# Performance work log

Hardware: AMD Instinct MI355X
Metric: run time of the kernel (lower is better)

## Reference

```python
import jax, jax.numpy as jnp
import numpy as np

B, N, KEY_DIM, VALUE_DIM, INNER_DIM, HEADS = 2, 4096, 512, 512, 512, 8
DIM_HEAD = INNER_DIM // HEADS
LN_EPS = 1e-5


def _layernorm(x, gamma, beta):
    mu = jnp.mean(x, axis=-1, keepdims=True)
    xc = x - mu
    var = jnp.mean(xc * xc, axis=-1, keepdims=True)
    return xc * jax.lax.rsqrt(var + LN_EPS) * gamma + beta


def setup_inputs() -> dict:
    key = jax.random.key(0)
    ks = jax.random.split(key, 8)
    keys = jax.random.normal(ks[0], (B, N, KEY_DIM), dtype=jnp.float32)
    values = jax.random.normal(ks[1], (B, N, VALUE_DIM), dtype=jnp.float32)
    mask = jax.random.randint(ks[2], (B, N), 0, 2).astype(jnp.bool_)
    W_qk = jax.random.normal(ks[3], (KEY_DIM, 2 * INNER_DIM), dtype=jnp.float32) * 0.02
    W_v = jax.random.normal(ks[4], (VALUE_DIM, INNER_DIM), dtype=jnp.float32) * 0.02
    W_out = jax.random.normal(ks[5], (INNER_DIM, VALUE_DIM), dtype=jnp.float32) * 0.02
    b_out = jnp.zeros((VALUE_DIM,), dtype=jnp.float32)
    qk_gamma = jnp.ones((KEY_DIM,), dtype=jnp.float32)
    qk_beta = jnp.zeros((KEY_DIM,), dtype=jnp.float32)
    v_gamma = jnp.ones((VALUE_DIM,), dtype=jnp.float32)
    v_beta = jnp.zeros((VALUE_DIM,), dtype=jnp.float32)
    return {"keys": keys, "values": values, "mask": mask,
            "qk_gamma": qk_gamma, "qk_beta": qk_beta,
            "v_gamma": v_gamma, "v_beta": v_beta,
            "W_qk": W_qk, "W_v": W_v, "W_out": W_out, "b_out": b_out}


def reference(keys, values, mask, qk_gamma, qk_beta, v_gamma, v_beta, W_qk, W_v, W_out, b_out):
    # LayerNorms on inputs
    kn = _layernorm(keys, qk_gamma, qk_beta)          # [B,N,KEY_DIM]
    vn = _layernorm(values, v_gamma, v_beta)          # [B,N,VALUE_DIM]
    # joint q/k projection, no bias
    qk = kn @ W_qk                                    # [B,N,2*INNER]
    q, k = qk[..., :INNER_DIM], qk[..., INNER_DIM:]
    # split heads: b n (h d) -> b h n d
    q = q.reshape(B, N, HEADS, DIM_HEAD).transpose(0, 2, 1, 3)
    k = k.reshape(B, N, HEADS, DIM_HEAD).transpose(0, 2, 1, 3)
    v = (vn @ W_v).reshape(B, N, HEADS, DIM_HEAD).transpose(0, 2, 1, 3)
    # clamp then scaled QK^T (AttentionMap math)
    q = jnp.clip(q, -5.0, 5.0)
    k = jnp.clip(k, -5.0, 5.0)
    scale = DIM_HEAD ** -0.5
    dots = jnp.einsum("bhqd,bhkd->bhqk", q, k) * scale  # [B,H,N,N]
    # mask: True keys are not attended to; broadcast (B,N)->(B,1,1,N)
    dots = jnp.where(mask[:, None, None, :], -jnp.inf, dots)
    attn = jax.nn.softmax(dots, axis=-1)
    out = jnp.einsum("bhqk,bhkd->bhqd", attn, v)       # [B,H,N,D]
    out = out.transpose(0, 2, 1, 3).reshape(B, N, INNER_DIM)
    return out @ W_out + b_out                         # [B,N,VALUE_DIM]
```

## Files before the change

kernel.cpp:

```cpp
#include <hip/hip_runtime.h>
#include <stdint.h>

typedef float f32x4 __attribute__((ext_vector_type(4)));
typedef float f32x16 __attribute__((ext_vector_type(16)));
typedef short s16x8 __attribute__((ext_vector_type(8)));
typedef int i32x4 __attribute__((ext_vector_type(4)));

typedef const __attribute__((address_space(1))) uint32_t* gas_t;
typedef __attribute__((address_space(3))) uint32_t* las_t;

__device__ __forceinline__ void gload16(const void* g, void* l) {
  __builtin_amdgcn_global_load_lds((gas_t)g, (las_t)l, 16, 0, 0);
}

__device__ __forceinline__ short f2bf(float f) {
  union { float f; uint32_t u; } v; v.f = f;
  uint32_t r = v.u + 0x7fffu + ((v.u >> 16) & 1u);
  return (short)(r >> 16);
}

__device__ __forceinline__ uint32_t cvtpk_bf16(float lo, float hi) {
  uint32_t r;
  asm("v_cvt_pk_bf16_f32 %0, %1, %2" : "=v"(r) : "v"(lo), "v"(hi));
  return r;
}

__device__ __forceinline__ void perm32swap(uint32_t& a, uint32_t& b) {
  asm("v_permlane32_swap_b32 %0, %1" : "+v"(a), "+v"(b));
}

#define MFMA16(a,b,c) __builtin_amdgcn_mfma_f32_16x16x32_bf16((a),(b),(c),0,0,0)
#define MFMA32(a,b,c) __builtin_amdgcn_mfma_f32_32x32x16_bf16((a),(b),(c),0,0,0)

__global__ void mask_detect_kernel(const uint32_t* __restrict__ m, uint32_t* __restrict__ flag) {
  uint32_t v = m[blockIdx.x * 256 + threadIdx.x];
  if (v > 1u) atomicOr(flag, 1u);
}

__global__ __launch_bounds__(256) void scan_kernel(const uint32_t* __restrict__ m,
    const uint32_t* __restrict__ flag, int* __restrict__ idx, int* __restrict__ cnts) {
  __shared__ int wt[4];
  const int b = blockIdx.x, t = threadIdx.x;
  const int lane = t & 63, w = t >> 6;
  const uint32_t f = *flag;
  int v[16]; int s = 0;
  if (f) {
    uint4 raw = ((const uint4*)((const uint8_t*)m + (size_t)b * 4096))[t];
    uint32_t ws_[4] = {raw.x, raw.y, raw.z, raw.w};
#pragma unroll
    for (int e = 0; e < 16; e++)
      v[e] = (((ws_[e >> 2] >> ((e & 3) * 8)) & 0xffu) == 0) ? 1 : 0;
  } else {
#pragma unroll
    for (int j = 0; j < 4; j++) {
      uint4 raw = ((const uint4*)(m + (size_t)b * 4096))[t * 4 + j];
      v[j * 4 + 0] = (raw.x == 0); v[j * 4 + 1] = (raw.y == 0);
      v[j * 4 + 2] = (raw.z == 0); v[j * 4 + 3] = (raw.w == 0);
    }
  }
#pragma unroll
  for (int e = 0; e < 16; e++) s += v[e];
  int sc = s;
#pragma unroll
  for (int off = 1; off < 64; off <<= 1) {
    int y = __shfl_up(sc, off);
    if (lane >= off) sc += y;
  }
  if (lane == 63) wt[w] = sc;
  __syncthreads();
  int woff = 0;
#pragma unroll
  for (int i = 0; i < 4; i++) if (i < w) woff += wt[i];
  int base = woff + sc - s;
#pragma unroll
  for (int e = 0; e < 16; e++)
    if (v[e]) { idx[b * 4096 + base] = b * 4096 + t * 16 + e; base++; }
  const int cnt = wt[0] + wt[1] + wt[2] + wt[3];
  const int cpad = (cnt + 127) & ~127;
  for (int j = cnt + t; j < cpad; j += 256) idx[b * 4096 + j] = 8192;
  if (t == 0) { cnts[b * 2] = cnt; cnts[b * 2 + 1] = cpad; }
}

__global__ __launch_bounds__(256) void transpose_kernel(const float* __restrict__ W,
    short* __restrict__ WT, int R, int C) {
  __shared__ float tile[32][33];
  const int c0 = blockIdx.x * 32, r0 = blockIdx.y * 32;
  const int tx = threadIdx.x & 31, ty = threadIdx.x >> 5;
#pragma unroll
  for (int i = 0; i < 32; i += 8)
    tile[ty + i][tx] = W[(size_t)(r0 + ty + i) * C + c0 + tx];
  __syncthreads();
#pragma unroll
  for (int i = 0; i < 32; i += 8)
    WT[(size_t)(c0 + ty + i) * R + r0 + tx] = f2bf(tile[tx][ty + i]);
}

__global__ __launch_bounds__(64) void ln_kernel(const float* __restrict__ keys,
    const float* __restrict__ values, const float* __restrict__ g0, const float* __restrict__ b0,
    const float* __restrict__ g1, const float* __restrict__ b1,
    short* __restrict__ kn, short* __restrict__ vn) {
  const int row = blockIdx.x, sel = blockIdx.y, lane = threadIdx.x;
  short* out = (sel ? vn : kn) + (size_t)row * 512;
  if (row == 8192) {
    s16x8 z = (s16x8){0,0,0,0,0,0,0,0};
    *(s16x8*)(out + lane * 8) = z;
    return;
  }
  const float* x = (sel ? values : keys) + (size_t)row * 512;
  const float* ga = sel ? g1 : g0;
  const float* be = sel ? b1 : b0;
  float4 a = ((const float4*)x)[lane * 2];
  float4 c = ((const float4*)x)[lane * 2 + 1];
  float s = a.x + a.y + a.z + a.w + c.x + c.y + c.z + c.w;
  float sq = a.x*a.x + a.y*a.y + a.z*a.z + a.w*a.w + c.x*c.x + c.y*c.y + c.z*c.z + c.w*c.w;
#pragma unroll
  for (int m = 1; m < 64; m <<= 1) { s += __shfl_xor(s, m); sq += __shfl_xor(sq, m); }
  float mu = s * (1.0f / 512.0f);
  float var = sq * (1.0f / 512.0f) - mu * mu;
  float rs = rsqrtf(var + 1e-5f);
  float xs[8] = {a.x, a.y, a.z, a.w, c.x, c.y, c.z, c.w};
  s16x8 o;
#pragma unroll
  for (int j = 0; j < 8; j++)
    o[j] = f2bf((xs[j] - mu) * rs * ga[lane * 8 + j] + be[lane * 8 + j]);
  *(s16x8*)(out + lane * 8) = o;
}

__device__ __forceinline__ void gemm_core(const short* __restrict__ A,
                                          const short* __restrict__ BT,
                                          int row0, int col0,
                                          short* ldsA, short* ldsB,
                                          f32x4 acc[4][4]) {
  const int t = threadIdx.x;
  const int lane = t & 63, w = t >> 6;
  const int wr = w >> 1, wc = w & 1;
  const int l15 = lane & 15, l4 = lane >> 4;
#pragma unroll
  for (int mi = 0; mi < 4; mi++)
#pragma unroll
    for (int ni = 0; ni < 4; ni++) acc[mi][ni] = (f32x4){0.f, 0.f, 0.f, 0.f};

  for (int k0 = 0; k0 < 512; k0 += 64) {
    __syncthreads();
#pragma unroll
    for (int i = 0; i < 4; i++) {
      int q = i * 256 + t;
      int row = q >> 3, ch = q & 7;
      int chs = ch ^ (row & 7);
      gload16(A + (size_t)(row0 + row) * 512 + k0 + chs * 8, ldsA + (i * 256 + w * 64) * 8);
      gload16(BT + (size_t)(col0 + row) * 512 + k0 + chs * 8, ldsB + (i * 256 + w * 64) * 8);
    }
    __syncthreads();
#pragma unroll
    for (int kk = 0; kk < 2; kk++) {
      s16x8 af[4], bf[4];
#pragma unroll
      for (int mi = 0; mi < 4; mi++) {
        int row = wr * 64 + mi * 16 + l15;
        int ch = (kk * 4 + l4) ^ (row & 7);
        af[mi] = *(const s16x8*)(ldsA + row * 64 + ch * 8);
      }
#pragma unroll
      for (int ni = 0; ni < 4; ni++) {
        int row = wc * 64 + ni * 16 + l15;
        int ch = (kk * 4 + l4) ^ (row & 7);
        bf[ni] = *(const s16x8*)(ldsB + row * 64 + ch * 8);
      }
#pragma unroll
      for (int mi = 0; mi < 4; mi++)
#pragma unroll
        for (int ni = 0; ni < 4; ni++)
          acc[mi][ni] = MFMA16(af[mi], bf[ni], acc[mi][ni]);
    }
  }
}

__device__ __forceinline__ void gemm_core64(const short* __restrict__ A,
                                            const short* __restrict__ BT,
                                            int row0, int col0,
                                            short* ldsA, short* ldsB,
                                            f32x4 acc[4][2]) {
  const int t = threadIdx.x;
  const int lane = t & 63, w = t >> 6;
  const int wr = w >> 1, wc = w & 1;
  const int l15 = lane & 15, l4 = lane >> 4;
#pragma unroll
  for (int mi = 0; mi < 4; mi++)
#pragma unroll
    for (int ni = 0; ni < 2; ni++) acc[mi][ni] = (f32x4){0.f, 0.f, 0.f, 0.f};

  for (int k0 = 0; k0 < 512; k0 += 64) {
    __syncthreads();
#pragma unroll
    for (int i = 0; i < 4; i++) {
      int q = i * 256 + t;
      int row = q >> 3, ch = q & 7;
      int chs = ch ^ (row & 7);
      gload16(A + (size_t)(row0 + row) * 512 + k0 + chs * 8, ldsA + (i * 256 + w * 64) * 8);
    }
#pragma unroll
    for (int i = 0; i < 2; i++) {
      int q = i * 256 + t;
      int row = q >> 3, ch = q & 7;
      int chs = ch ^ (row & 7);
      gload16(BT + (size_t)(col0 + row) * 512 + k0 + chs * 8, ldsB + (i * 256 + w * 64) * 8);
    }
    __syncthreads();
#pragma unroll
    for (int kk = 0; kk < 2; kk++) {
      s16x8 af[4], bf[2];
#pragma unroll
      for (int mi = 0; mi < 4; mi++) {
        int row = wr * 64 + mi * 16 + l15;
        int ch = (kk * 4 + l4) ^ (row & 7);
        af[mi] = *(const s16x8*)(ldsA + row * 64 + ch * 8);
      }
#pragma unroll
      for (int ni = 0; ni < 2; ni++) {
        int row = wc * 32 + ni * 16 + l15;
        int ch = (kk * 4 + l4) ^ (row & 7);
        bf[ni] = *(const s16x8*)(ldsB + row * 64 + ch * 8);
      }
#pragma unroll
      for (int mi = 0; mi < 4; mi++)
#pragma unroll
        for (int ni = 0; ni < 2; ni++)
          acc[mi][ni] = MFMA16(af[mi], bf[ni], acc[mi][ni]);
    }
  }
}

__device__ __forceinline__ void gemm_core_idx(const short* __restrict__ A,
                                              const short* __restrict__ BT,
                                              const int* __restrict__ idxp,
                                              int row0, int col0,
                                              short* ldsA, short* ldsB,
                                              f32x4 acc[4][4]) {
  const int t = threadIdx.x;
  const int lane = t & 63, w = t >> 6;
  const int wr = w >> 1, wc = w & 1;
  const int l15 = lane & 15, l4 = lane >> 4;
  int arow[4];
#pragma unroll
  for (int i = 0; i < 4; i++)
    arow[i] = idxp[row0 + ((i * 256 + t) >> 3)];
#pragma unroll
  for (int mi = 0; mi < 4; mi++)
#pragma unroll
    for (int ni = 0; ni < 4; ni++) acc[mi][ni] = (f32x4){0.f, 0.f, 0.f, 0.f};

  for (int k0 = 0; k0 < 512; k0 += 64) {
    __syncthreads();
#pragma unroll
    for (int i = 0; i < 4; i++) {
      int q = i * 256 + t;
      int row = q >> 3, ch = q & 7;
      int chs = ch ^ (row & 7);
      gload16(A + (size_t)arow[i] * 512 + k0 + chs * 8, ldsA + (i * 256 + w * 64) * 8);
      gload16(BT + (size_t)(col0 + row) * 512 + k0 + chs * 8, ldsB + (i * 256 + w * 64) * 8);
    }
    __syncthreads();
#pragma unroll
    for (int kk = 0; kk < 2; kk++) {
      s16x8 af[4], bf[4];
#pragma unroll
      for (int mi = 0; mi < 4; mi++) {
        int row = wr * 64 + mi * 16 + l15;
        int ch = (kk * 4 + l4) ^ (row & 7);
        af[mi] = *(const s16x8*)(ldsA + row * 64 + ch * 8);
      }
#pragma unroll
      for (int ni = 0; ni < 4; ni++) {
        int row = wc * 64 + ni * 16 + l15;
        int ch = (kk * 4 + l4) ^ (row & 7);
        bf[ni] = *(const s16x8*)(ldsB + row * 64 + ch * 8);
      }
#pragma unroll
      for (int mi = 0; mi < 4; mi++)
#pragma unroll
        for (int ni = 0; ni < 4; ni++)
          acc[mi][ni] = MFMA16(af[mi], bf[ni], acc[mi][ni]);
    }
  }
}

__global__ __launch_bounds__(256) void gemm_q_kernel(const short* __restrict__ kn,
    const short* __restrict__ WqkT, short* __restrict__ Qg) {
  __shared__ short ldsA[128 * 64], ldsB[64 * 64];
  f32x4 acc[4][2];
  const int bm = blockIdx.x, bn = blockIdx.y;
  gemm_core64(kn, WqkT, bm * 128, bn * 64, ldsA, ldsB, acc);
  const int t = threadIdx.x, lane = t & 63, w = t >> 6, wr = w >> 1, wc = w & 1;
  const int l15 = lane & 15, l4 = lane >> 4;
  const float QSCL = 0.125f * 1.44269504088896f;
#pragma unroll
  for (int mi = 0; mi < 4; mi++)
#pragma unroll
    for (int ni = 0; ni < 2; ni++) {
      int c = bn * 64 + wc * 32 + ni * 16 + l15;
      int h = c >> 6, d = c & 63;
#pragma unroll
      for (int r = 0; r < 4; r++) {
        int row = bm * 128 + wr * 64 + mi * 16 + l4 * 4 + r;
        int b = row >> 12, n = row & 4095;
        float v = acc[mi][ni][r];
        v = fminf(fmaxf(v, -5.0f), 5.0f) * QSCL;
        Qg[((size_t)((b * 8 + h) * 4096 + n) << 6) + d] = f2bf(v);
      }
    }
}

__global__ __launch_bounds__(256) void gemm_kv_kernel(const short* __restrict__ kn,
    const short* __restrict__ vn, const short* __restrict__ WqkT,
    const short* __restrict__ WvT, const int* __restrict__ idx,
    const int* __restrict__ cnts, short* __restrict__ Kg, short* __restrict__ VTg) {
  const int z = blockIdx.z, b = z & 1, isV = z >> 1;
  const int bm = blockIdx.x, bn = blockIdx.y;
  if (bm * 128 >= cnts[b * 2 + 1]) return;
  __shared__ short lds[2][128 * 64];
  f32x4 acc[4][4];
  const int t = threadIdx.x, lane = t & 63, w = t >> 6, wr = w >> 1, wc = w & 1;
  const int l15 = lane & 15, l4 = lane >> 4;
  if (!isV) {
    gemm_core_idx(kn, WqkT, idx + b * 4096, bm * 128, 512 + bn * 128, lds[0], lds[1], acc);
#pragma unroll
    for (int mi = 0; mi < 4; mi++)
#pragma unroll
      for (int ni = 0; ni < 4; ni++) {
        int c = bn * 128 + wc * 64 + ni * 16 + l15;
        int h = c >> 6, d = c & 63;
#pragma unroll
        for (int r = 0; r < 4; r++) {
          int j = bm * 128 + wr * 64 + mi * 16 + l4 * 4 + r;
          float v = acc[mi][ni][r];
          v = fminf(fmaxf(v, -5.0f), 5.0f);
          Kg[((size_t)((b * 8 + h) * 4096 + j) << 6) + d] = f2bf(v);
        }
      }
  } else {
    gemm_core_idx(vn, WvT, idx + b * 4096, bm * 128, bn * 128, lds[0], lds[1], acc);
    __syncthreads();
    short* T = (short*)lds;
#pragma unroll
    for (int mi = 0; mi < 4; mi++)
#pragma unroll
      for (int ni = 0; ni < 4; ni++) {
        int c_loc = wc * 64 + ni * 16 + l15;
#pragma unroll
        for (int r = 0; r < 4; r++) {
          int n_loc = wr * 64 + mi * 16 + l4 * 4 + r;
          T[c_loc * 128 + (((n_loc >> 3) ^ (c_loc & 15)) << 3) + (n_loc & 7)] = f2bf(acc[mi][ni][r]);
        }
      }
    __syncthreads();
#pragma unroll
    for (int jj = 0; jj < 8; jj++) {
      int c_loc = jj * 16 + (t >> 4);
      int nch = t & 15;
      s16x8 v = *(const s16x8*)(T + c_loc * 128 + ((nch ^ (c_loc & 15)) << 3));
      int cg = bn * 128 + c_loc, h = cg >> 6, d = cg & 63;
      int j = bm * 128 + nch * 8;
      *(s16x8*)(VTg + (size_t)((b * 8 + h) * 64 + d) * 4096 + j) = v;
    }
  }
}

__global__ __launch_bounds__(256) void gemm_out_kernel(const short* __restrict__ O,
    const short* __restrict__ WoutT, const float* __restrict__ bias, float* __restrict__ out) {
  __shared__ short ldsA[128 * 64], ldsB[64 * 64];
  f32x4 acc[4][2];
  const int bm = blockIdx.x, bn = blockIdx.y;
  gemm_core64(O, WoutT, bm * 128, bn * 64, ldsA, ldsB, acc);
  const int t = threadIdx.x, lane = t & 63, w = t >> 6, wr = w >> 1, wc = w & 1;
  const int l15 = lane & 15, l4 = lane >> 4;
#pragma unroll
  for (int ni = 0; ni < 2; ni++) {
    int col = bn * 64 + wc * 32 + ni * 16 + l15;
    float bv = bias[col];
#pragma unroll
    for (int mi = 0; mi < 4; mi++)
#pragma unroll
      for (int r = 0; r < 4; r++) {
        int row = bm * 128 + wr * 64 + mi * 16 + l4 * 4 + r;
        out[(size_t)row * 512 + col] = acc[mi][ni][r] + bv;
      }
  }
}

__global__ __launch_bounds__(512, 4) void attn_kernel(const short* __restrict__ Qg,
    const short* __restrict__ Kg, const short* __restrict__ VTg,
    const int* __restrict__ cnts, short* __restrict__ O) {
  __shared__ short smem[32768];
  short* KloB = smem;
  short* VloB = smem + 8192;
  short* KhiB = smem + 16384;
  short* VhiB = smem + 24576;

  const int bid = blockIdx.x;
  const int xcd = bid & 7, local = bid >> 3;
  const int bh = xcd * 2 + (local & 1);
  const int qb = local >> 1;
  const int b = bh >> 3, h = bh & 7;
  const int t = threadIdx.x, lane = t & 63, w = t >> 6;
  const int l31 = lane & 31, hh = lane >> 5;
  const int half = w >> 2, wq = w & 3;

  const short* Qp = Qg + (size_t)bh * 4096 * 64;
  const short* Kp = Kg + (size_t)bh * 4096 * 64;
  const short* Vp = VTg + (size_t)bh * 64 * 4096;

  const int cnt  = cnts[b * 2];
  const int cpad = cnts[b * 2 + 1];
  const int nit  = cpad >> 7;
  const int hb   = cpad >> 1;
  const int kbase = half ? hb : 0;

  const int qrow = qb * 128 + wq * 32 + l31;
  s16x8 qf[4];
#pragma unroll
  for (int dblk = 0; dblk < 4; dblk++)
    qf[dblk] = *(const s16x8*)(Qp + (size_t)qrow * 64 + dblk * 16 + hh * 8);

  f32x16 oac[2];
#pragma unroll
  for (int db = 0; db < 2; db++)
#pragma unroll
    for (int r = 0; r < 16; r++) oac[db][r] = 0.0f;
  float m_ = -60.0f, l_ = 0.0f;

  const short* KtS = half ? KhiB : KloB;
  const short* VtS = half ? VhiB : VloB;

  auto STAGE = [&](int buf, int i) {
    int row = t >> 3, ch = t & 7, chs = ch ^ (row & 7);
    gload16(Kp + (size_t)(i * 64 + row) * 64 + chs * 8,        KloB + buf * 4096 + w * 512);
    gload16(Kp + (size_t)(hb + i * 64 + row) * 64 + chs * 8,   KhiB + buf * 4096 + w * 512);
    gload16(Vp + (size_t)row * 4096 + i * 64 + chs * 8,        VloB + buf * 4096 + w * 512);
    gload16(Vp + (size_t)row * 4096 + hb + i * 64 + chs * 8,   VhiB + buf * 4096 + w * 512);
  };

  STAGE(0, 0);
  __syncthreads();

  for (int it = 0; it < nit; it++) {
    const int cur = it & 1;
    if (it < nit - 1) STAGE(cur ^ 1, it + 1);
    const short* Kt = KtS + cur * 4096;
    const int kb_t = kbase + it * 64;

    f32x16 sc[2];
    __builtin_amdgcn_s_setprio(1);
#pragma unroll
    for (int kb = 0; kb < 2; kb++) {
      f32x16 s_;
#pragma unroll
      for (int r = 0; r < 16; r++) s_[r] = 0.0f;
      const int krow = kb * 32 + l31;
#pragma unroll
      for (int dblk = 0; dblk < 4; dblk++) {
        int ch = (2 * dblk + hh) ^ (krow & 7);
        s16x8 kf = *(const s16x8*)(Kt + krow * 64 + ch * 8);
        s_ = MFMA32(kf, qf[dblk], s_);
      }
      sc[kb] = s_;
    }
    __builtin_amdgcn_s_setprio(0);

    if (kb_t + 64 > cnt) {
#pragma unroll
      for (int kb = 0; kb < 2; kb++)
#pragma unroll
        for (int r = 0; r < 16; r++) {
          int key = kb_t + kb * 32 + (r & 3) + 8 * (r >> 2) + 4 * hh;
          if (key >= cnt) sc[kb][r] = -1e30f;
        }
    }

    float mx0 = -1e30f, mx1 = -1e30f, mx2 = -1e30f, mx3 = -1e30f;
#pragma unroll
    for (int kb = 0; kb < 2; kb++)
#pragma unroll
      for (int r = 0; r < 16; r += 4) {
        mx0 = fmaxf(mx0, sc[kb][r + 0]);
        mx1 = fmaxf(mx1, sc[kb][r + 1]);
        mx2 = fmaxf(mx2, sc[kb][r + 2]);
        mx3 = fmaxf(mx3, sc[kb][r + 3]);
      }
    float mx = fmaxf(fmaxf(mx0, mx1), fmaxf(mx2, mx3));
    mx = fmaxf(mx, __shfl_xor(mx, 32));

    if (!__all(mx <= m_ + 5.0f)) {
      float mnew = fmaxf(m_, mx);
      float alpha = __builtin_amdgcn_exp2f(m_ - mnew);
      m_ = mnew;
      l_ *= alpha;
#pragma unroll
      for (int db = 0; db < 2; db++)
#pragma unroll
        for (int r = 0; r < 16; r++) oac[db][r] *= alpha;
    }

    float ls = 0.0f;
    uint32_t pw[4][4];
#pragma unroll
    for (int kb = 0; kb < 2; kb++) {
      float p[16];
#pragma unroll
      for (int r = 0; r < 16; r++) {
        p[r] = __builtin_amdgcn_exp2f(sc[kb][r] - m_);
        ls += p[r];
      }
#pragma unroll
      for (int ksl = 0; ksl < 2; ksl++) {
        const int fi = kb * 2 + ksl, b0 = ksl * 8;
        uint32_t a0 = cvtpk_bf16(p[b0 + 0], p[b0 + 1]);
        uint32_t b0w = cvtpk_bf16(p[b0 + 4], p[b0 + 5]);
        perm32swap(a0, b0w);
        uint32_t a1 = cvtpk_bf16(p[b0 + 2], p[b0 + 3]);
        uint32_t b1w = cvtpk_bf16(p[b0 + 6], p[b0 + 7]);
        perm32swap(a1, b1w);
        pw[fi][0] = a0; pw[fi][1] = a1; pw[fi][2] = b0w; pw[fi][3] = b1w;
      }
    }
    ls += __shfl_xor(ls, 32);
    l_ += ls;

    __builtin_amdgcn_s_setprio(1);
#pragma unroll
    for (int db = 0; db < 2; db++) {
      const int d = db * 32 + l31;
#pragma unroll
      for (int ks = 0; ks < 4; ks++) {
        int ch = (2 * ks + hh) ^ (d & 7);
        s16x8 vf = *(const s16x8*)(VtS + cur * 4096 + d * 64 + ch * 8);
        i32x4 pv = {(int)pw[ks][0], (int)pw[ks][1], (int)pw[ks][2], (int)pw[ks][3]};
        oac[db] = MFMA32(vf, __builtin_bit_cast(s16x8, pv), oac[db]);
      }
    }
    __builtin_amdgcn_s_setprio(0);

    __syncthreads();
  }

  float* mrg = (float*)smem;
  float* ml  = mrg + 8192;
  if (half) {
#pragma unroll
    for (int db = 0; db < 2; db++)
#pragma unroll
      for (int r = 0; r < 16; r++)
        mrg[wq * 2048 + (db * 16 + r) * 64 + lane] = oac[db][r];
    ml[wq * 128 + lane * 2]     = m_;
    ml[wq * 128 + lane * 2 + 1] = l_;
  }
  __syncthreads();
  if (!half) {
    float m2 = ml[wq * 128 + lane * 2];
    float l2 = ml[wq * 128 + lane * 2 + 1];
    float mF = fmaxf(m_, m2);
    float e1 = __builtin_amdgcn_exp2f(m_ - mF);
    float e2 = __builtin_amdgcn_exp2f(m2 - mF);
    l_ = l_ * e1 + l2 * e2;
#pragma unroll
    for (int db = 0; db < 2; db++)
#pragma unroll
      for (int r = 0; r < 16; r++)
        oac[db][r] = oac[db][r] * e1 + mrg[wq * 2048 + (db * 16 + r) * 64 + lane] * e2;

    float inv = 1.0f / l_;
    short* epi = smem + 17408 + wq * 2048;
#pragma unroll
    for (int db = 0; db < 2; db++)
#pragma unroll
      for (int g = 0; g < 4; g++) {
        uint32_t w0 = cvtpk_bf16(oac[db][g * 4 + 0] * inv, oac[db][g * 4 + 1] * inv);
        uint32_t w1 = cvtpk_bf16(oac[db][g * 4 + 2] * inv, oac[db][g * 4 + 3] * inv);
        int chunk = db * 4 + g;
        uint2* dst = (uint2*)((char*)epi + l31 * 128 + ((chunk ^ (l31 & 7)) << 4) + hh * 8);
        *dst = make_uint2(w0, w1);
      }
#pragma unroll
    for (int i = 0; i < 4; i++) {
      int c = hh * 4 + i;
      s16x8 v = *(const s16x8*)((char*)epi + l31 * 128 + ((c ^ (l31 & 7)) << 4));
      *(s16x8*)(O + ((size_t)(b * 4096 + qrow) * 512) + h * 64 + c * 8) = v;
    }
  }
}

extern "C" void kernel_launch(void* const* d_in, const int* in_sizes, int n_in,
                              void* d_out, int out_size, void* d_ws, size_t ws_size,
                              hipStream_t stream) {
  const float* keys     = (const float*)d_in[0];
  const float* values   = (const float*)d_in[1];
  const uint32_t* maskp = (const uint32_t*)d_in[2];
  const float* qk_gamma = (const float*)d_in[3];
  const float* qk_beta  = (const float*)d_in[4];
  const float* v_gamma  = (const float*)d_in[5];
  const float* v_beta   = (const float*)d_in[6];
  const float* W_qk     = (const float*)d_in[7];
  const float* W_v      = (const float*)d_in[8];
  const float* W_out    = (const float*)d_in[9];
  const float* b_out    = (const float*)d_in[10];
  float* out = (float*)d_out;
  char* ws = (char*)d_ws;
  const size_t MB = 1u << 20;
  short* kn    = (short*)(ws);
  short* vn    = (short*)(ws + 9 * MB);
  short* Qg    = (short*)(ws + 18 * MB);
  short* Kg    = (short*)(ws + 26 * MB);
  short* VTg   = (short*)(ws + 34 * MB);
  short* O     = (short*)(ws + 42 * MB);
  short* WqkT  = (short*)(ws + 50 * MB);
  short* WvT   = (short*)(ws + 51 * MB);
  short* WoutT = (short*)(ws + 51 * MB + 512 * 1024);
  int*   idx   = (int*)(ws + 52 * MB);
  int*   cnts  = (int*)(ws + 52 * MB + 32 * 1024);
  uint32_t* flag = (uint32_t*)(ws + 52 * MB + 33 * 1024);

  hipMemsetAsync(flag, 0, 4, stream);
  mask_detect_kernel<<<8, 256, 0, stream>>>(maskp, flag);
  scan_kernel<<<2, 256, 0, stream>>>(maskp, flag, idx, cnts);
  transpose_kernel<<<dim3(32, 16), 256, 0, stream>>>(W_qk, WqkT, 512, 1024);
  transpose_kernel<<<dim3(16, 16), 256, 0, stream>>>(W_v, WvT, 512, 512);
  transpose_kernel<<<dim3(16, 16), 256, 0, stream>>>(W_out, WoutT, 512, 512);
  ln_kernel<<<dim3(8193, 2), 64, 0, stream>>>(keys, values, qk_gamma, qk_beta, v_gamma, v_beta, kn, vn);
  gemm_q_kernel<<<dim3(64, 8), 256, 0, stream>>>(kn, WqkT, Qg);
  gemm_kv_kernel<<<dim3(32, 4, 4), 256, 0, stream>>>(kn, vn, WqkT, WvT, idx, cnts, Kg, VTg);
  attn_kernel<<<512, 512, 0, stream>>>(Qg, Kg, VTg, cnts, O);
  gemm_out_kernel<<<dim3(64, 8), 256, 0, stream>>>(O, WoutT, b_out, out);
}
```

Before: 110.8 us.

## Merge prep launches into one kernel and fuse Q/KV projection kernels

Folds mask detection, the mask scan, the three weight transposes and both LayerNorms into a single prep_kernel launch that dispatches on block index. LayerNorm rows are now handled by four waves per 256-thread block instead of one 64-thread block each. Mask-type detection becomes a per-block ballot in place of a memset plus an atomic kernel. The Q projection and the masked K/V projections share one proj_kernel launch. The goal is to cut launch count and inter-kernel gaps, at the cost of a heterogeneous grid whose branches have different register and LDS needs.

```diff
diff --git a/kernel.cpp b/kernel.cpp
--- a/kernel.cpp
+++ b/kernel.cpp
@@ -32,146 +32,111 @@
 #define MFMA16(a,b,c) __builtin_amdgcn_mfma_f32_16x16x32_bf16((a),(b),(c),0,0,0)
 #define MFMA32(a,b,c) __builtin_amdgcn_mfma_f32_32x32x16_bf16((a),(b),(c),0,0,0)
 
-__global__ void mask_detect_kernel(const uint32_t* __restrict__ m, uint32_t* __restrict__ flag) {
-  uint32_t v = m[blockIdx.x * 256 + threadIdx.x];
-  if (v > 1u) atomicOr(flag, 1u);
-}
-
-__global__ __launch_bounds__(256) void scan_kernel(const uint32_t* __restrict__ m,
-    const uint32_t* __restrict__ flag, int* __restrict__ idx, int* __restrict__ cnts) {
+__global__ __launch_bounds__(256) void prep_kernel(
+    const uint32_t* __restrict__ maskp,
+    const float* __restrict__ W_qk, const float* __restrict__ W_v,
+    const float* __restrict__ W_out,
+    short* __restrict__ WqkT, short* __restrict__ WvT, short* __restrict__ WoutT,
+    const float* __restrict__ keys, const float* __restrict__ values,
+    const float* __restrict__ g0, const float* __restrict__ b0,
+    const float* __restrict__ g1, const float* __restrict__ b1,
+    short* __restrict__ kn, short* __restrict__ vn,
+    int* __restrict__ idx, int* __restrict__ cnts) {
+  __shared__ float tile[32][33];
   __shared__ int wt[4];
-  const int b = blockIdx.x, t = threadIdx.x;
+  __shared__ int wdet[4];
+  const int bid = blockIdx.x, t = threadIdx.x;
   const int lane = t & 63, w = t >> 6;
-  const uint32_t f = *flag;
-  int v[16]; int s = 0;
-  if (f) {
-    uint4 raw = ((const uint4*)((const uint8_t*)m + (size_t)b * 4096))[t];
-    uint32_t ws_[4] = {raw.x, raw.y, raw.z, raw.w};
+
+  if (bid < 2) {
+    const int b = bid;
+    uint4 probe = ((const uint4*)maskp)[t];
+    bool big = (probe.x > 1u) || (probe.y > 1u) || (probe.z > 1u) || (probe.w > 1u);
+    unsigned long long bal = __ballot(big);
+    if (lane == 0) wdet[w] = (bal != 0ull) ? 1 : 0;
+    __syncthreads();
+    const int f = wdet[0] | wdet[1] | wdet[2] | wdet[3];
+
+    int v[16]; int s = 0;
+    if (f) {
+      uint4 raw = ((const uint4*)((const uint8_t*)maskp + (size_t)b * 4096))[t];
+      uint32_t ws_[4] = {raw.x, raw.y, raw.z, raw.w};
+#pragma unroll
+      for (int e = 0; e < 16; e++)
+        v[e] = (((ws_[e >> 2] >> ((e & 3) * 8)) & 0xffu) == 0) ? 1 : 0;
+    } else {
+#pragma unroll
+      for (int j = 0; j < 4; j++) {
+        uint4 raw = ((const uint4*)(maskp + (size_t)b * 4096))[t * 4 + j];
+        v[j * 4 + 0] = (raw.x == 0); v[j * 4 + 1] = (raw.y == 0);
+        v[j * 4 + 2] = (raw.z == 0); v[j * 4 + 3] = (raw.w == 0);
+      }
+    }
+#pragma unroll
+    for (int e = 0; e < 16; e++) s += v[e];
+    int sc = s;
+#pragma unroll
+    for (int off = 1; off < 64; off <<= 1) {
+      int y = __shfl_up(sc, off);
+      if (lane >= off) sc += y;
+    }
+    if (lane == 63) wt[w] = sc;
+    __syncthreads();
+    int woff = 0;
+#pragma unroll
+    for (int i = 0; i < 4; i++) if (i < w) woff += wt[i];
+    int base = woff + sc - s;
 #pragma unroll
     for (int e = 0; e < 16; e++)
-      v[e] = (((ws_[e >> 2] >> ((e & 3) * 8)) & 0xffu) == 0) ? 1 : 0;
+      if (v[e]) { idx[b * 4096 + base] = b * 4096 + t * 16 + e; base++; }
+    const int cnt = wt[0] + wt[1] + wt[2] + wt[3];
+    const int cpad = (cnt + 127) & ~127;
+    for (int j = cnt + t; j < cpad; j += 256) idx[b * 4096 + j] = 8192;
+    if (t == 0) { cnts[b * 2] = cnt; cnts[b * 2 + 1] = cpad; }
+  } else if (bid < 1026) {
+    int job = bid - 2;
+    const float* W; short* WT; int C;
+    if (job < 512)       { W = W_qk;  WT = WqkT;  C = 1024; }
+    else if (job < 768)  { job -= 512; W = W_v;   WT = WvT;  C = 512; }
+    else                 { job -= 768; W = W_out; WT = WoutT; C = 512; }
+    const int tx_ = C >> 5;
+    const int c0 = (job % tx_) * 32, r0 = (job / tx_) * 32;
+    const int tx = t & 31, ty = t >> 5;
+#pragma unroll
+    for (int i = 0; i < 32; i += 8)
+      tile[ty + i][tx] = W[(size_t)(r0 + ty + i) * C + c0 + tx];
+    __syncthreads();
+#pragma unroll
+    for (int i = 0; i < 32; i += 8)
+      WT[(size_t)(c0 + ty + i) * 512 + r0 + tx] = f2bf(tile[tx][ty + i]);
   } else {
-#pragma unroll
-    for (int j = 0; j < 4; j++) {
-      uint4 raw = ((const uint4*)(m + (size_t)b * 4096))[t * 4 + j];
-      v[j * 4 + 0] = (raw.x == 0); v[j * 4 + 1] = (raw.y == 0);
-      v[j * 4 + 2] = (raw.z == 0); v[j * 4 + 3] = (raw.w == 0);
-    }
-  }
-#pragma unroll
-  for (int e = 0; e < 16; e++) s += v[e];
-  int sc = s;
-#pragma unroll
-  for (int off = 1; off < 64; off <<= 1) {
-    int y = __shfl_up(sc, off);
-    if (lane >= off) sc += y;
-  }
-  if (lane == 63) wt[w] = sc;
-  __syncthreads();
-  int woff = 0;
-#pragma unroll
-  for (int i = 0; i < 4; i++) if (i < w) woff += wt[i];
-  int base = woff + sc - s;
-#pragma unroll
-  for (int e = 0; e < 16; e++)
-    if (v[e]) { idx[b * 4096 + base] = b * 4096 + t * 16 + e; base++; }
-  const int cnt = wt[0] + wt[1] + wt[2] + wt[3];
-  const int cpad = (cnt + 127) & ~127;
-  for (int j = cnt + t; j < cpad; j += 256) idx[b * 4096 + j] = 8192;
-  if (t == 0) { cnts[b * 2] = cnt; cnts[b * 2 + 1] = cpad; }
-}
-
-__global__ __launch_bounds__(256) void transpose_kernel(const float* __restrict__ W,
-    short* __restrict__ WT, int R, int C) {
-  __shared__ float tile[32][33];
-  const int c0 = blockIdx.x * 32, r0 = blockIdx.y * 32;
-  const int tx = threadIdx.x & 31, ty = threadIdx.x >> 5;
-#pragma unroll
-  for (int i = 0; i < 32; i += 8)
-    tile[ty + i][tx] = W[(size_t)(r0 + ty + i) * C + c0 + tx];
-  __syncthreads();
-#pragma unroll
-  for (int i = 0; i < 32; i += 8)
-    WT[(size_t)(c0 + ty + i) * R + r0 + tx] = f2bf(tile[tx][ty + i]);
-}
-
-__global__ __launch_bounds__(64) void ln_kernel(const float* __restrict__ keys,
-    const float* __restrict__ values, const float* __restrict__ g0, const float* __restrict__ b0,
-    const float* __restrict__ g1, const float* __restrict__ b1,
-    short* __restrict__ kn, short* __restrict__ vn) {
-  const int row = blockIdx.x, sel = blockIdx.y, lane = threadIdx.x;
-  short* out = (sel ? vn : kn) + (size_t)row * 512;
-  if (row == 8192) {
-    s16x8 z = (s16x8){0,0,0,0,0,0,0,0};
-    *(s16x8*)(out + lane * 8) = z;
-    return;
-  }
-  const float* x = (sel ? values : keys) + (size_t)row * 512;
-  const float* ga = sel ? g1 : g0;
-  const float* be = sel ? b1 : b0;
-  float4 a = ((const float4*)x)[lane * 2];
-  float4 c = ((const float4*)x)[lane * 2 + 1];
-  float s = a.x + a.y + a.z + a.w + c.x + c.y + c.z + c.w;
-  float sq = a.x*a.x + a.y*a.y + a.z*a.z + a.w*a.w + c.x*c.x + c.y*c.y + c.z*c.z + c.w*c.w;
-#pragma unroll
-  for (int m = 1; m < 64; m <<= 1) { s += __shfl_xor(s, m); sq += __shfl_xor(sq, m); }
-  float mu = s * (1.0f / 512.0f);
-  float var = sq * (1.0f / 512.0f) - mu * mu;
-  float rs = rsqrtf(var + 1e-5f);
-  float xs[8] = {a.x, a.y, a.z, a.w, c.x, c.y, c.z, c.w};
-  s16x8 o;
-#pragma unroll
-  for (int j = 0; j < 8; j++)
-    o[j] = f2bf((xs[j] - mu) * rs * ga[lane * 8 + j] + be[lane * 8 + j]);
-  *(s16x8*)(out + lane * 8) = o;
-}
-
-__device__ __forceinline__ void gemm_core(const short* __restrict__ A,
-                                          const short* __restrict__ BT,
-                                          int row0, int col0,
-                                          short* ldsA, short* ldsB,
-                                          f32x4 acc[4][4]) {
-  const int t = threadIdx.x;
-  const int lane = t & 63, w = t >> 6;
-  const int wr = w >> 1, wc = w & 1;
-  const int l15 = lane & 15, l4 = lane >> 4;
-#pragma unroll
-  for (int mi = 0; mi < 4; mi++)
-#pragma unroll
-    for (int ni = 0; ni < 4; ni++) acc[mi][ni] = (f32x4){0.f, 0.f, 0.f, 0.f};
-
-  for (int k0 = 0; k0 < 512; k0 += 64) {
-    __syncthreads();
-#pragma unroll
-    for (int i = 0; i < 4; i++) {
-      int q = i * 256 + t;
-      int row = q >> 3, ch = q & 7;
-      int chs = ch ^ (row & 7);
-      gload16(A + (size_t)(row0 + row) * 512 + k0 + chs * 8, ldsA + (i * 256 + w * 64) * 8);
-      gload16(BT + (size_t)(col0 + row) * 512 + k0 + chs * 8, ldsB + (i * 256 + w * 64) * 8);
-    }
-    __syncthreads();
-#pragma unroll
-    for (int kk = 0; kk < 2; kk++) {
-      s16x8 af[4], bf[4];
-#pragma unroll
-      for (int mi = 0; mi < 4; mi++) {
-        int row = wr * 64 + mi * 16 + l15;
-        int ch = (kk * 4 + l4) ^ (row & 7);
-        af[mi] = *(const s16x8*)(ldsA + row * 64 + ch * 8);
-      }
-#pragma unroll
-      for (int ni = 0; ni < 4; ni++) {
-        int row = wc * 64 + ni * 16 + l15;
-        int ch = (kk * 4 + l4) ^ (row & 7);
-        bf[ni] = *(const s16x8*)(ldsB + row * 64 + ch * 8);
-      }
-#pragma unroll
-      for (int mi = 0; mi < 4; mi++)
-#pragma unroll
-        for (int ni = 0; ni < 4; ni++)
-          acc[mi][ni] = MFMA16(af[mi], bf[ni], acc[mi][ni]);
-    }
+    int job = (bid - 1026) * 4 + w;
+    if (job >= 16386) return;
+    const int sel = job & 1, row = job >> 1;
+    short* out = (sel ? vn : kn) + (size_t)row * 512;
+    if (row == 8192) {
+      s16x8 z = (s16x8){0,0,0,0,0,0,0,0};
+      *(s16x8*)(out + lane * 8) = z;
+      return;
+    }
+    const float* x = (sel ? values : keys) + (size_t)row * 512;
+    const float* ga = sel ? g1 : g0;
+    const float* be = sel ? b1 : b0;
+    float4 a = ((const float4*)x)[lane * 2];
+    float4 c = ((const float4*)x)[lane * 2 + 1];
+    float s = a.x + a.y + a.z + a.w + c.x + c.y + c.z + c.w;
+    float sq = a.x*a.x + a.y*a.y + a.z*a.z + a.w*a.w + c.x*c.x + c.y*c.y + c.z*c.z + c.w*c.w;
+#pragma unroll
+    for (int m = 1; m < 64; m <<= 1) { s += __shfl_xor(s, m); sq += __shfl_xor(sq, m); }
+    float mu = s * (1.0f / 512.0f);
+    float var = sq * (1.0f / 512.0f) - mu * mu;
+    float rs = rsqrtf(var + 1e-5f);
+    float xs[8] = {a.x, a.y, a.z, a.w, c.x, c.y, c.z, c.w};
+    s16x8 o;
+#pragma unroll
+    for (int j = 0; j < 8; j++)
+      o[j] = f2bf((xs[j] - mu) * rs * ga[lane * 8 + j] + be[lane * 8 + j]);
+    *(s16x8*)(out + lane * 8) = o;
   }
 }
 
@@ -284,83 +249,83 @@
   }
 }
 
-__global__ __launch_bounds__(256) void gemm_q_kernel(const short* __restrict__ kn,
-    const short* __restrict__ WqkT, short* __restrict__ Qg) {
-  __shared__ short ldsA[128 * 64], ldsB[64 * 64];
-  f32x4 acc[4][2];
-  const int bm = blockIdx.x, bn = blockIdx.y;
-  gemm_core64(kn, WqkT, bm * 128, bn * 64, ldsA, ldsB, acc);
+__global__ __launch_bounds__(256) void proj_kernel(const short* __restrict__ kn,
+    const short* __restrict__ vn, const short* __restrict__ WqkT,
+    const short* __restrict__ WvT, const int* __restrict__ idx,
+    const int* __restrict__ cnts, short* __restrict__ Qg,
+    short* __restrict__ Kg, short* __restrict__ VTg) {
+  __shared__ short lds[2][128 * 64];
+  const int bid = blockIdx.x;
   const int t = threadIdx.x, lane = t & 63, w = t >> 6, wr = w >> 1, wc = w & 1;
   const int l15 = lane & 15, l4 = lane >> 4;
-  const float QSCL = 0.125f * 1.44269504088896f;
-#pragma unroll
-  for (int mi = 0; mi < 4; mi++)
-#pragma unroll
-    for (int ni = 0; ni < 2; ni++) {
-      int c = bn * 64 + wc * 32 + ni * 16 + l15;
-      int h = c >> 6, d = c & 63;
-#pragma unroll
-      for (int r = 0; r < 4; r++) {
-        int row = bm * 128 + wr * 64 + mi * 16 + l4 * 4 + r;
-        int b = row >> 12, n = row & 4095;
-        float v = acc[mi][ni][r];
-        v = fminf(fmaxf(v, -5.0f), 5.0f) * QSCL;
-        Qg[((size_t)((b * 8 + h) * 4096 + n) << 6) + d] = f2bf(v);
-      }
-    }
-}
-
-__global__ __launch_bounds__(256) void gemm_kv_kernel(const short* __restrict__ kn,
-    const short* __restrict__ vn, const short* __restrict__ WqkT,
-    const short* __restrict__ WvT, const int* __restrict__ idx,
-    const int* __restrict__ cnts, short* __restrict__ Kg, short* __restrict__ VTg) {
-  const int z = blockIdx.z, b = z & 1, isV = z >> 1;
-  const int bm = blockIdx.x, bn = blockIdx.y;
-  if (bm * 128 >= cnts[b * 2 + 1]) return;
-  __shared__ short lds[2][128 * 64];
-  f32x4 acc[4][4];
-  const int t = threadIdx.x, lane = t & 63, w = t >> 6, wr = w >> 1, wc = w & 1;
-  const int l15 = lane & 15, l4 = lane >> 4;
-  if (!isV) {
-    gemm_core_idx(kn, WqkT, idx + b * 4096, bm * 128, 512 + bn * 128, lds[0], lds[1], acc);
+
+  if (bid < 512) {
+    const int bm = bid >> 3, bn = bid & 7;
+    f32x4 acc[4][2];
+    gemm_core64(kn, WqkT, bm * 128, bn * 64, lds[0], lds[1], acc);
+    const float QSCL = 0.125f * 1.44269504088896f;
 #pragma unroll
     for (int mi = 0; mi < 4; mi++)
 #pragma unroll
-      for (int ni = 0; ni < 4; ni++) {
-        int c = bn * 128 + wc * 64 + ni * 16 + l15;
+      for (int ni = 0; ni < 2; ni++) {
+        int c = bn * 64 + wc * 32 + ni * 16 + l15;
         int h = c >> 6, d = c & 63;
 #pragma unroll
         for (int r = 0; r < 4; r++) {
-          int j = bm * 128 + wr * 64 + mi * 16 + l4 * 4 + r;
+          int row = bm * 128 + wr * 64 + mi * 16 + l4 * 4 + r;
+          int b = row >> 12, n = row & 4095;
           float v = acc[mi][ni][r];
-          v = fminf(fmaxf(v, -5.0f), 5.0f);
-          Kg[((size_t)((b * 8 + h) * 4096 + j) << 6) + d] = f2bf(v);
+          v = fminf(fmaxf(v, -5.0f), 5.0f) * QSCL;
+          Qg[((size_t)((b * 8 + h) * 4096 + n) << 6) + d] = f2bf(v);
         }
       }
   } else {
-    gemm_core_idx(vn, WvT, idx + b * 4096, bm * 128, bn * 128, lds[0], lds[1], acc);
-    __syncthreads();
-    short* T = (short*)lds;
-#pragma unroll
-    for (int mi = 0; mi < 4; mi++)
-#pragma unroll
-      for (int ni = 0; ni < 4; ni++) {
-        int c_loc = wc * 64 + ni * 16 + l15;
-#pragma unroll
-        for (int r = 0; r < 4; r++) {
-          int n_loc = wr * 64 + mi * 16 + l4 * 4 + r;
-          T[c_loc * 128 + (((n_loc >> 3) ^ (c_loc & 15)) << 3) + (n_loc & 7)] = f2bf(acc[mi][ni][r]);
+    const int b2 = bid - 512;
+    const int bm = b2 >> 4, bn = (b2 >> 2) & 3, z = b2 & 3;
+    const int b = z & 1, isV = z >> 1;
+    if (bm * 128 >= cnts[b * 2 + 1]) return;
+    f32x4 acc[4][4];
+    if (!isV) {
+      gemm_core_idx(kn, WqkT, idx + b * 4096, bm * 128, 512 + bn * 128, lds[0], lds[1], acc);
+#pragma unroll
+      for (int mi = 0; mi < 4; mi++)
+#pragma unroll
+        for (int ni = 0; ni < 4; ni++) {
+          int c = bn * 128 + wc * 64 + ni * 16 + l15;
+          int h = c >> 6, d = c & 63;
+#pragma unroll
+          for (int r = 0; r < 4; r++) {
+            int j = bm * 128 + wr * 64 + mi * 16 + l4 * 4 + r;
+            float v = acc[mi][ni][r];
+            v = fminf(fmaxf(v, -5.0f), 5.0f);
+            Kg[((size_t)((b * 8 + h) * 4096 + j) << 6) + d] = f2bf(v);
+          }
         }
-      }
-    __syncthreads();
-#pragma unroll
-    for (int jj = 0; jj < 8; jj++) {
-      int c_loc = jj * 16 + (t >> 4);
-      int nch = t & 15;
-      s16x8 v = *(const s16x8*)(T + c_loc * 128 + ((nch ^ (c_loc & 15)) << 3));
-      int cg = bn * 128 + c_loc, h = cg >> 6, d = cg & 63;
-      int j = bm * 128 + nch * 8;
-      *(s16x8*)(VTg + (size_t)((b * 8 + h) * 64 + d) * 4096 + j) = v;
+    } else {
+      gemm_core_idx(vn, WvT, idx + b * 4096, bm * 128, bn * 128, lds[0], lds[1], acc);
+      __syncthreads();
+      short* T = (short*)lds;
+#pragma unroll
+      for (int mi = 0; mi < 4; mi++)
+#pragma unroll
+        for (int ni = 0; ni < 4; ni++) {
+          int c_loc = wc * 64 + ni * 16 + l15;
+#pragma unroll
+          for (int r = 0; r < 4; r++) {
+            int n_loc = wr * 64 + mi * 16 + l4 * 4 + r;
+            T[c_loc * 128 + (((n_loc >> 3) ^ (c_loc & 15)) << 3) + (n_loc & 7)] = f2bf(acc[mi][ni][r]);
+          }
+        }
+      __syncthreads();
+#pragma unroll
+      for (int jj = 0; jj < 8; jj++) {
+        int c_loc = jj * 16 + (t >> 4);
+        int nch = t & 15;
+        s16x8 v = *(const s16x8*)(T + c_loc * 128 + ((nch ^ (c_loc & 15)) << 3));
+        int cg = bn * 128 + c_loc, h = cg >> 6, d = cg & 63;
+        int j = bm * 128 + nch * 8;
+        *(s16x8*)(VTg + (size_t)((b * 8 + h) * 64 + d) * 4096 + j) = v;
+      }
     }
   }
 }
@@ -616,17 +581,11 @@
   short* WoutT = (short*)(ws + 51 * MB + 512 * 1024);
   int*   idx   = (int*)(ws + 52 * MB);
   int*   cnts  = (int*)(ws + 52 * MB + 32 * 1024);
-  uint32_t* flag = (uint32_t*)(ws + 52 * MB + 33 * 1024);
-
-  hipMemsetAsync(flag, 0, 4, stream);
-  mask_detect_kernel<<<8, 256, 0, stream>>>(maskp, flag);
-  scan_kernel<<<2, 256, 0, stream>>>(maskp, flag, idx, cnts);
-  transpose_kernel<<<dim3(32, 16), 256, 0, stream>>>(W_qk, WqkT, 512, 1024);
-  transpose_kernel<<<dim3(16, 16), 256, 0, stream>>>(W_v, WvT, 512, 512);
-  transpose_kernel<<<dim3(16, 16), 256, 0, stream>>>(W_out, WoutT, 512, 512);
-  ln_kernel<<<dim3(8193, 2), 64, 0, stream>>>(keys, values, qk_gamma, qk_beta, v_gamma, v_beta, kn, vn);
-  gemm_q_kernel<<<dim3(64, 8), 256, 0, stream>>>(kn, WqkT, Qg);
-  gemm_kv_kernel<<<dim3(32, 4, 4), 256, 0, stream>>>(kn, vn, WqkT, WvT, idx, cnts, Kg, VTg);
+
+  prep_kernel<<<5123, 256, 0, stream>>>(maskp, W_qk, W_v, W_out, WqkT, WvT, WoutT,
+                                        keys, values, qk_gamma, qk_beta, v_gamma, v_beta,
+                                        kn, vn, idx, cnts);
+  proj_kernel<<<1024, 256, 0, stream>>>(kn, vn, WqkT, WvT, idx, cnts, Qg, Kg, VTg);
   attn_kernel<<<512, 512, 0, stream>>>(Qg, Kg, VTg, cnts, O);
   gemm_out_kernel<<<dim3(64, 8), 256, 0, stream>>>(O, WoutT, b_out, out);
 }
```

After: 95.80 us. 13.6% less time.
